# Kernel tuning notes

Hardware: AMD Instinct MI355X
Metric: run time of the kernel (lower is better)

Reference implementation:

```python
import jax, jax.numpy as jnp
import numpy as np
import math

SHIFTS = (1, 2, 4, 8)
EPS_IN = 1e-5  # InstanceNorm2d eps
EPS_BN = 1e-5  # BatchNorm2d eps

def _eight_shifts(x, d):
    # Reproduces DATrans.feature_padding: 8 reflection-padded shifted views.
    H, W = x.shape[-2], x.shape[-1]
    def p(rt, rb, cl, cr):
        return jnp.pad(x, ((0, 0), (0, 0), (rt, rb), (cl, cr)), mode='reflect')
    return [
        p(d, 0, d, 0)[..., :H, :W],   # left-top
        p(d, 0, 0, 0)[..., :H, :],    # center-top
        p(d, 0, 0, d)[..., :H, d:],   # right-top
        p(0, 0, d, 0)[..., :, :W],    # left-center
        p(0, 0, 0, d)[..., :, d:],    # right-center
        p(0, d, d, 0)[..., d:, :W],   # left-bottom
        p(0, d, 0, 0)[..., d:, :],    # center-bottom
        p(0, d, 0, d)[..., d:, d:],   # right-bottom
    ]

def _l2n(x):
    # torch F.normalize(dim=-1, eps=1e-12)
    return x / jnp.maximum(jnp.linalg.norm(x, axis=-1, keepdims=True), 1e-12)

def setup_inputs() -> dict:
    key = jax.random.key(0)
    ks = jax.random.split(key, 9)
    B, Cin, H, W = 4, 16, 256, 256
    heads, hidden, NL, Cout = 4, 16, 8, 16
    tra = heads * hidden
    cen = jax.random.normal(ks[0], (B, Cin, H, W), jnp.float32)
    q_w = jax.random.normal(ks[1], (heads, hidden, Cin), jnp.float32) / np.sqrt(Cin).astype(np.float32)
    k_w = jax.random.normal(ks[2], (heads, hidden * NL, Cin * NL), jnp.float32) / np.sqrt(Cin * NL).astype(np.float32)
    v_w = jax.random.normal(ks[3], (heads, hidden * NL, Cin * NL), jnp.float32) / np.sqrt(Cin * NL).astype(np.float32)
    out_w = jax.random.normal(ks[4], (Cout, tra), jnp.float32) / np.sqrt(tra).astype(np.float32)
    bn_gamma = jax.random.uniform(ks[5], (Cout,), jnp.float32) + 0.5
    bn_beta = jax.random.normal(ks[6], (Cout,), jnp.float32) * 0.1
    bn_mean = jax.random.normal(ks[7], (Cout,), jnp.float32) * 0.1
    bn_var = jax.random.uniform(ks[8], (Cout,), jnp.float32) + 0.5
    return dict(cen=cen, q_w=q_w, k_w=k_w, v_w=v_w, out_w=out_w,
                bn_gamma=bn_gamma, bn_beta=bn_beta, bn_mean=bn_mean, bn_var=bn_var)

def reference(cen, q_w, k_w, v_w, out_w, bn_gamma, bn_beta, bn_mean, bn_var):
    b, Cin, H, W = cen.shape
    area = H * W
    heads = len(SHIFTS)
    qs, ksl, vsl = [], [], []
    for i, d in enumerate(SHIFTS):  # small fixed loop over heads
        sur = jnp.concatenate([s - cen for s in _eight_shifts(cen, d)], axis=1)  # [b, 8*Cin, H, W]
        ksl.append(jnp.einsum('oc,bchw->bohw', k_w[i], sur))  # 1x1 conv, no bias
        vsl.append(jnp.einsum('oc,bchw->bohw', v_w[i], sur))
        qs.append(jnp.einsum('oc,bchw->bohw', q_w[i], cen))
    # torch stack(dim=2).view(b, heads, -1, area) on contiguous tensor == stack+reshape
    K = jnp.stack(ksl, axis=2).reshape(b, heads, -1, area)  # [b, heads, 8*hid, area]
    Q = jnp.stack(qs, axis=2).reshape(b, heads, -1, area)   # [b, heads, hid, area]
    V = jnp.stack(vsl, axis=2).reshape(b, heads, -1, area)
    scores = jnp.einsum('bhca,bhda->bhcd', _l2n(Q), _l2n(K)) / math.sqrt(area)  # [b,h,hid,8*hid]
    # InstanceNorm2d(heads): per (b, head) over last two dims, no affine
    mu = scores.mean(axis=(-2, -1), keepdims=True)
    var = scores.var(axis=(-2, -1), keepdims=True)
    attn = jax.nn.softmax((scores - mu) * jax.lax.rsqrt(var + EPS_IN), axis=-1)
    out = jnp.einsum('bhcd,bhda->bhca', attn, V)  # [b, heads, hid, area]
    tra = out.shape[1] * out.shape[2]
    out = out.reshape(b, tra, H, W)
    out = jnp.einsum('oc,bchw->bohw', out_w, out)  # out_conv 1x1, no bias
    g = bn_gamma[None, :, None, None]
    bta = bn_beta[None, :, None, None]
    m = bn_mean[None, :, None, None]
    v = bn_var[None, :, None, None]
    out = (out - m) * jax.lax.rsqrt(v + EPS_BN) * g + bta  # eval-mode BatchNorm2d
    return jax.nn.relu(out)
```

## Files before the change

### kernel.cpp

```cpp
#include <hip/hip_runtime.h>
#include <math.h>

#define HH 256
#define WW 256
#define AREA 65536
#define CIN 16
#define NS 4
#define CSUR 128
#define NEXT 144
#define NPAIR 45

typedef __attribute__((ext_vector_type(8))) _Float16 f16x8;
typedef __attribute__((ext_vector_type(4))) float f32x4;

__constant__ int c_dy[8] = {-1,-1,-1, 0, 0, 1, 1, 1};
__constant__ int c_dx[8] = {-1, 0, 1,-1, 1,-1, 0, 1};

__device__ constexpr int CTI[NPAIR] = {
    0, 1,1, 2,2,2, 3,3,3,3, 4,4,4,4,4,
    5,5,5,5,5,5, 6,6,6,6,6,6,6, 7,7,7,7,7,7,7,7,
    8,8,8,8,8,8,8,8,8};
__device__ constexpr int CTJ[NPAIR] = {
    0, 0,1, 0,1,2, 0,1,2,3, 0,1,2,3,4,
    0,1,2,3,4,5, 0,1,2,3,4,5,6, 0,1,2,3,4,5,6,7,
    0,1,2,3,4,5,6,7,8};

__device__ __forceinline__ int refl(int v) {
    return v < 0 ? -v : (v > 255 ? 510 - v : v);
}

__device__ __forceinline__ unsigned pkh(float a, float b) {
    auto h2 = __builtin_amdgcn_cvt_pkrtz(a, b);
    return __builtin_bit_cast(unsigned, h2);
}

__device__ __forceinline__ void wph(unsigned* __restrict__ m,
                                    int c, int pxp, int halfk, float a, float b) {
    const int sw = c & 7, gi = halfk * 4 + (pxp >> 2), e = pxp & 3;
    m[c * 32 + ((gi ^ sw) << 2) + e] = pkh(a, b);
}

template <bool FAST>
__device__ __forceinline__ void stage64(unsigned* __restrict__ m,
                                        const float* __restrict__ base,
                                        int y, int x0, int cin, int pxp, int d) {
    constexpr int DY[8] = {-1,-1,-1, 0, 0, 1, 1, 1};
    constexpr int DX[8] = {-1, 0, 1,-1, 1,-1, 0, 1};
    const int xA = x0 + 2 * pxp;
    const int xB = xA + 32;
    const float* rowy = base + y * WW;
    const float2 cA = *(const float2*)(rowy + xA);
    const float2 cB = *(const float2*)(rowy + xB);
    wph(m, cin, pxp, 0, cA.x, cA.y);
    wph(m, cin, pxp, 1, cB.x, cB.y);
#pragma unroll
    for (int kk = 0; kk < 8; ++kk) {
        float2 sA, sB;
        if (FAST) {
            const float* row = base + (y + DY[kk] * d) * WW;
            sA = *(const float2*)(row + xA + DX[kk] * d);
            sB = *(const float2*)(row + xB + DX[kk] * d);
        } else {
            const int ys = refl(y + DY[kk] * d);
            const float* row = base + ys * WW;
            const int off = DX[kk] * d;
            sA.x = row[refl(xA + off)];
            sA.y = row[refl(xA + 1 + off)];
            sB.x = row[refl(xB + off)];
            sB.y = row[refl(xB + 1 + off)];
        }
        const int c = 16 + kk * 16 + cin;
        wph(m, c, pxp, 0, sA.x - cA.x, sA.y - cA.y);
        wph(m, c, pxp, 1, sB.x - cB.x, sB.y - cB.y);
    }
}

__global__ __launch_bounds__(256) void k1_gram(const float* __restrict__ cen,
                                               float* __restrict__ part) {
    const int chunk = blockIdx.x;
    const int s = blockIdx.y;
    const int b = blockIdx.z;
    const int d = 1 << s;
    const int t = threadIdx.x;
    const int lane = t & 63, wid = t >> 6;
    const int lr = lane & 15, lg = lane >> 4;
    const int cin = t >> 4, pxp = t & 15;
    const int y0 = chunk * 4;
    const float* base = cen + ((size_t)b * CIN + cin) * AREA;

    __shared__ unsigned lds[NEXT * 32];

    const int rA = ((lg ^ (lr & 7)) << 2);
    const int rB = (((4 + lg) ^ (lr & 7)) << 2);

    f32x4 acc[12];
#pragma unroll
    for (int i = 0; i < 12; ++i) acc[i] = (f32x4){0.f, 0.f, 0.f, 0.f};

    for (int rd = 0; rd < 16; ++rd) {
        const int y  = y0 + (rd >> 2);
        const int x0 = (rd & 3) * 64;
        if (y >= 8 && y <= 247 && x0 >= 64 && x0 <= 128)
            stage64<true>(lds, base, y, x0, cin, pxp, d);
        else
            stage64<false>(lds, base, y, x0, cin, pxp, d);
        __syncthreads();
        f16x8 fA[9], fB[9];
#pragma unroll
        for (int tt = 0; tt < 9; ++tt) {
            const int rb = (tt * 16 + lr) * 32;
            fA[tt] = __builtin_bit_cast(f16x8, *(const uint4*)(lds + rb + rA));
            fB[tt] = __builtin_bit_cast(f16x8, *(const uint4*)(lds + rb + rB));
        }
        __syncthreads();
#pragma unroll
        for (int p = 0; p < NPAIR; ++p) {
            if ((p & 3) == wid) {
                const int i = CTI[p], j = CTJ[p], a = p >> 2;
                acc[a] = __builtin_amdgcn_mfma_f32_16x16x32_f16(fA[i], fA[j], acc[a], 0, 0, 0);
                acc[a] = __builtin_amdgcn_mfma_f32_16x16x32_f16(fB[i], fB[j], acc[a], 0, 0, 0);
            }
        }
    }

    float* tb = part + (size_t)((chunk & 3) * 16 + b * 4 + s) * 20736;
#pragma unroll
    for (int p = 0; p < NPAIR; ++p) {
        if ((p & 3) == wid) {
            const int gi0 = CTI[p] * 16 + lg * 4;
            const int gj  = CTJ[p] * 16 + lr;
            const f32x4 a = acc[p >> 2];
#pragma unroll
            for (int r = 0; r < 4; ++r)
                atomicAdd(&tb[(gi0 + r) * 144 + gj], a[r]);
        }
    }
}

__global__ __launch_bounds__(256) void kA(const float* __restrict__ part,
                                          const float* __restrict__ q_w,
                                          const float* __restrict__ k_w,
                                          float* __restrict__ A,
                                          float* __restrict__ normK,
                                          float* __restrict__ normQ) {
    const int s = blockIdx.x, b = blockIdx.y, z = blockIdx.z, bs = b * 4 + s;
    const int t = threadIdx.x;
    const int i0 = z * 16;
    __shared__ float Ts[16][148];
    __shared__ float kwS[128][129];
    __shared__ float red[2][128];

    const float* p0 = part + (size_t)(0 * 16 + bs) * 20736;
    const float* p1 = part + (size_t)(1 * 16 + bs) * 20736;
    const float* p2 = part + (size_t)(2 * 16 + bs) * 20736;
    const float* p3 = part + (size_t)(3 * 16 + bs) * 20736;
    for (int e = t; e < 16 * 144; e += 256) {
        const int il = e / 144, j = e - il * 144;
        const int i = i0 + il;
        const int src = (i >= j) ? (i * 144 + j) : (j * 144 + i);
        Ts[il][j] = p0[src] + p1[src] + p2[src] + p3[src];
    }
    if (z >= 1) {
        const float* kws = k_w + (size_t)s * 16384;
        for (int e = t; e < 16384; e += 256)
            kwS[e >> 7][e & 127] = kws[e];
    }
    __syncthreads();

    if (z >= 1) {
        for (int e = t; e < 1024; e += 256) {
            const int il = e >> 6, jq = e & 63;
            const float* qr = q_w + jq * 16;
            float aa = 0.f;
#pragma unroll
            for (int c = 0; c < 16; ++c) aa = fmaf(qr[c], Ts[il][c], aa);
            A[((size_t)bs * 64 + jq) * 128 + (i0 - 16 + il)] = aa;
        }
        const int ck = t & 127, half = t >> 7;
        float accil[16];
#pragma unroll
        for (int il = 0; il < 16; ++il) accil[il] = 0.f;
        for (int j = half * 64; j < half * 64 + 64; ++j) {
            const float kj = kwS[ck][j];
#pragma unroll
            for (int il = 0; il < 16; ++il)
                accil[il] = fmaf(kj, Ts[il][16 + j], accil[il]);
        }
        float prt = 0.f;
#pragma unroll
        for (int il = 0; il < 16; ++il)
            prt = fmaf(kwS[ck][i0 - 16 + il], accil[il], prt);
        red[half][ck] = prt;
        __syncthreads();
        if (t < 128)
            atomicAdd(&normK[(size_t)bs * 128 + t], red[0][t] + red[1][t]);
    } else if (s == 0 && t < 64) {
        float nq = 0.f;
#pragma unroll
        for (int c1 = 0; c1 < 16; ++c1) {
            float ra = 0.f;
#pragma unroll
            for (int c2 = 0; c2 < 16; ++c2)
                ra = fmaf(q_w[t * 16 + c2], Ts[c1][c2], ra);
            nq = fmaf(q_w[t * 16 + c1], ra, nq);
        }
        normQ[b * 64 + t] = nq;
    }
}

__global__ __launch_bounds__(256) void kB(const float* __restrict__ k_w,
                                          const float* __restrict__ v_w,
                                          const float* __restrict__ A,
                                          const float* __restrict__ normK,
                                          const float* __restrict__ normQ,
                                          float* __restrict__ wEff) {
    const int a = blockIdx.x, b = blockIdx.y;
    const int t = threadIdx.x;
    __shared__ float AS[4][16][128];
    __shared__ float kv[4][32][132];
    __shared__ float sc[2048];
    __shared__ float red[256];
    __shared__ float rowred[256];
    __shared__ float rowmax[16], rowsum[16];
    __shared__ float s_mu, s_rs;

    for (int idx = t; idx < 8192; idx += 256) {
        const int sk = idx >> 11, rr = (idx >> 7) & 15, cp = idx & 127;
        const int jq = (rr & 3) * 16 + 4 * a + (rr >> 2);
        AS[sk][rr][cp] = A[((size_t)(b * 4 + sk) * 64 + jq) * 128 + cp];
    }
    for (int idx = t; idx < 16384; idx += 256) {
        const int sk = idx >> 12, ckl = (idx >> 7) & 31, cp = idx & 127;
        kv[sk][ckl][cp] = k_w[((size_t)sk * 128 + 32 * a + ckl) * 128 + cp];
    }
    __syncthreads();
    for (int e = t; e < 2048; e += 256) {
        const int r = e >> 7, dd = e & 127;
        const int sk = dd & 3, ckl = dd >> 2;
        const float4* Ar = (const float4*)(&AS[sk][r][0]);
        const float4* kr = (const float4*)(&kv[sk][ckl][0]);
        float4 pv = {0.f, 0.f, 0.f, 0.f};
#pragma unroll 8
        for (int jj = 0; jj < 32; ++jj) {
            const float4 h = Ar[jj], k4 = kr[jj];
            pv.x = fmaf(h.x, k4.x, pv.x);
            pv.y = fmaf(h.y, k4.y, pv.y);
            pv.z = fmaf(h.z, k4.z, pv.z);
            pv.w = fmaf(h.w, k4.w, pv.w);
        }
        const float dot = pv.x + pv.y + pv.z + pv.w;
        const int jq = (r & 3) * 16 + 4 * a + (r >> 2);
        const float qn = fmaxf(sqrtf(fmaxf(normQ[b * 64 + jq], 0.f)), 1e-12f);
        const float kn = fmaxf(sqrtf(fmaxf(normK[(size_t)(b * 4 + sk) * 128 + 32 * a + ckl], 0.f)), 1e-12f);
        sc[e] = dot / (qn * kn * 256.0f);
    }
    __syncthreads();
    for (int idx = t; idx < 16384; idx += 256) {
        const int sk = idx >> 12, m = (idx >> 7) & 31, cp = idx & 127;
        kv[sk][m][cp] = v_w[((size_t)sk * 128 + 32 * a + m) * 128 + cp];
    }
    {
        float p = 0.f;
        for (int e = t; e < 2048; e += 256) p += sc[e];
        red[t] = p; __syncthreads();
        for (int off = 128; off > 0; off >>= 1) {
            if (t < off) red[t] += red[t + off];
            __syncthreads();
        }
        if (t == 0) s_mu = red[0] * (1.f / 2048.f);
        __syncthreads();
    }
    {
        const float mu = s_mu;
        float p = 0.f;
        for (int e = t; e < 2048; e += 256) { const float z = sc[e] - mu; p += z * z; }
        red[t] = p; __syncthreads();
        for (int off = 128; off > 0; off >>= 1) {
            if (t < off) red[t] += red[t + off];
            __syncthreads();
        }
        if (t == 0) s_rs = rsqrtf(red[0] * (1.f / 2048.f) + 1e-5f);
        __syncthreads();
    }
    const float mu = s_mu, rs = s_rs;
    const int r = t >> 4, l = t & 15;
    {
        float m = -1e30f;
#pragma unroll
        for (int j = 0; j < 8; ++j) {
            const float z = (sc[r * 128 + l + j * 16] - mu) * rs;
            m = fmaxf(m, z);
        }
        rowred[t] = m; __syncthreads();
        if (l == 0) {
            float m2 = rowred[r * 16];
            for (int j = 1; j < 16; ++j) m2 = fmaxf(m2, rowred[r * 16 + j]);
            rowmax[r] = m2;
        }
        __syncthreads();
    }
    {
        float p = 0.f;
#pragma unroll
        for (int j = 0; j < 8; ++j) {
            const float z = (sc[r * 128 + l + j * 16] - mu) * rs;
            p += expf(z - rowmax[r]);
        }
        rowred[t] = p; __syncthreads();
        if (l == 0) {
            float p2 = 0.f;
            for (int j = 0; j < 16; ++j) p2 += rowred[r * 16 + j];
            rowsum[r] = p2;
        }
        __syncthreads();
    }
    {
        float vals[8];
#pragma unroll
        for (int j = 0; j < 8; ++j) {
            const float z = (sc[r * 128 + l + j * 16] - mu) * rs;
            vals[j] = expf(z - rowmax[r]) / rowsum[r];
        }
        __syncthreads();
#pragma unroll
        for (int j = 0; j < 8; ++j) sc[r * 128 + l + j * 16] = vals[j];
        __syncthreads();
    }
    for (int e = t; e < 8192; e += 256) {
        const int sk = e >> 11, r2 = (e >> 7) & 15, cp = e & 127;
        float w = 0.f;
#pragma unroll
        for (int m = 0; m < 32; ++m)
            w = fmaf(sc[r2 * 128 + 4 * m + sk], kv[sk][m][cp], w);
        wEff[((size_t)(b * 4 + sk) * 64 + (a * 16 + r2)) * 128 + cp] = w;
    }
}

__global__ __launch_bounds__(256) void k2c(const float* __restrict__ out_w,
                                           const float* __restrict__ bn_gamma,
                                           const float* __restrict__ bn_var,
                                           const float* __restrict__ wEff,
                                           float* __restrict__ wFinT,
                                           float* __restrict__ wcG) {
    const int s = blockIdx.x, b = blockIdx.y;
    const int t = threadIdx.x;
    __shared__ float we[64][128];
    __shared__ float wfS[16][128];
    for (int idx = t; idx < 8192; idx += 256) {
        const int j = idx >> 7, cp = idx & 127;
        we[j][cp] = wEff[((size_t)(b * 4 + s) * 64 + j) * 128 + cp];
    }
    __syncthreads();
    for (int e = t; e < 2048; e += 256) {
        const int o = e >> 7, cp = e & 127;
        float w = 0.f;
#pragma unroll 16
        for (int j = 0; j < 64; ++j)
            w = fmaf(out_w[o * 64 + j], we[j][cp], w);
        const float scale = bn_gamma[o] * rsqrtf(bn_var[o] + 1e-5f);
        const float wv = w * scale;
        wfS[o][cp] = wv;
        wFinT[((size_t)(b * 4 + s) * 128 + cp) * 16 + o] = wv;
    }
    __syncthreads();
    {
        const int cin = t >> 4, o = t & 15;
        float p = 0.f;
#pragma unroll
        for (int kk = 0; kk < 8; ++kk) p += wfS[o][kk * 16 + cin];
        atomicAdd(&wcG[(size_t)b * 256 + cin * 16 + o], p);
    }
}

__global__ __launch_bounds__(256) void k3_out(const float* __restrict__ cen,
                                              const float* __restrict__ wFinT,
                                              const float* __restrict__ wcG,
                                              const float* __restrict__ bn_gamma,
                                              const float* __restrict__ bn_beta,
                                              const float* __restrict__ bn_mean,
                                              const float* __restrict__ bn_var,
                                              float* __restrict__ out) {
    const int y = blockIdx.x;
    const int b = blockIdx.y;
    const int x = threadIdx.x;
    const float* cb = cen + (size_t)b * CIN * AREA;

    float acc[16];
#pragma unroll
    for (int o = 0; o < 16; ++o) acc[o] = 0.f;

    for (int s = 0; s < NS; ++s) {
        const int d = 1 << s;
        for (int k = 0; k < 8; ++k) {
            const int ry = refl(y + c_dy[k] * d);
            const int rx = refl(x + c_dx[k] * d);
            const float* crow = cb + ry * WW;
            const int woff = __builtin_amdgcn_readfirstlane(
                ((b * 4 + s) * 128 + k * 16) * 16);
            const float* wbase = wFinT + woff;
#pragma unroll
            for (int cin = 0; cin < 16; ++cin) {
                const float v = crow[cin * AREA + rx];
                const float4* w4 = reinterpret_cast<const float4*>(wbase + cin * 16);
#pragma unroll
                for (int oq = 0; oq < 4; ++oq) {
                    const float4 w = w4[oq];
                    acc[oq*4+0] = fmaf(w.x, v, acc[oq*4+0]);
                    acc[oq*4+1] = fmaf(w.y, v, acc[oq*4+1]);
                    acc[oq*4+2] = fmaf(w.z, v, acc[oq*4+2]);
                    acc[oq*4+3] = fmaf(w.w, v, acc[oq*4+3]);
                }
            }
        }
    }
    {
        const float* crow = cb + y * WW;
        const int coff = __builtin_amdgcn_readfirstlane(b * 256);
        const float* wcb = wcG + coff;
#pragma unroll
        for (int cin = 0; cin < 16; ++cin) {
            const float v = crow[cin * AREA + x];
            const float4* w4 = reinterpret_cast<const float4*>(wcb + cin * 16);
#pragma unroll
            for (int oq = 0; oq < 4; ++oq) {
                const float4 w = w4[oq];
                acc[oq*4+0] = fmaf(-w.x, v, acc[oq*4+0]);
                acc[oq*4+1] = fmaf(-w.y, v, acc[oq*4+1]);
                acc[oq*4+2] = fmaf(-w.z, v, acc[oq*4+2]);
                acc[oq*4+3] = fmaf(-w.w, v, acc[oq*4+3]);
            }
        }
    }
#pragma unroll
    for (int o = 0; o < 16; ++o) {
        const float scale = bn_gamma[o] * rsqrtf(bn_var[o] + 1e-5f);
        const float bias  = bn_beta[o] - bn_mean[o] * scale;
        out[((size_t)(b * 16 + o) * HH + y) * WW + x] = fmaxf(acc[o] + bias, 0.f);
    }
}

extern "C" void kernel_launch(void* const* d_in, const int* in_sizes, int n_in,
                              void* d_out, int out_size, void* d_ws, size_t ws_size,
                              hipStream_t stream) {
    const float* cen      = (const float*)d_in[0];
    const float* q_w      = (const float*)d_in[1];
    const float* k_w      = (const float*)d_in[2];
    const float* v_w      = (const float*)d_in[3];
    const float* out_w    = (const float*)d_in[4];
    const float* bn_gamma = (const float*)d_in[5];
    const float* bn_beta  = (const float*)d_in[6];
    const float* bn_mean  = (const float*)d_in[7];
    const float* bn_var   = (const float*)d_in[8];
    float* out = (float*)d_out;

    char* ws = (char*)d_ws;
    const size_t PART_BYTES  = (size_t)4 * 16 * 20736 * 4;
    const size_t NK_BYTES    = (size_t)16 * 128 * 4;
    const size_t WC_BYTES    = (size_t)4 * 256 * 4;
    const size_t A_BYTES     = (size_t)16 * 64 * 128 * 4;
    const size_t NQ_BYTES    = (size_t)4 * 64 * 4;
    const size_t WEFF_BYTES  = (size_t)16 * 64 * 128 * 4;

    float* part  = (float*)(ws);
    float* normK = (float*)(ws + PART_BYTES);
    float* wcG   = (float*)(ws + PART_BYTES + NK_BYTES);
    float* A     = (float*)(ws + PART_BYTES + NK_BYTES + WC_BYTES);
    float* normQ = (float*)(ws + PART_BYTES + NK_BYTES + WC_BYTES + A_BYTES);
    float* wEff  = (float*)(ws + PART_BYTES + NK_BYTES + WC_BYTES + A_BYTES + NQ_BYTES);
    float* wFinT = (float*)(ws + PART_BYTES + NK_BYTES + WC_BYTES + A_BYTES + NQ_BYTES + WEFF_BYTES);

    (void)hipMemsetAsync(part, 0, PART_BYTES + NK_BYTES + WC_BYTES, stream);
    k1_gram<<<dim3(64, 4, 4), 256, 0, stream>>>(cen, part);
    kA<<<dim3(4, 4, 9), 256, 0, stream>>>(part, q_w, k_w, A, normK, normQ);
    kB<<<dim3(4, 4), 256, 0, stream>>>(k_w, v_w, A, normK, normQ, wEff);
    k2c<<<dim3(4, 4), 256, 0, stream>>>(out_w, bn_gamma, bn_var, wEff, wFinT, wcG);
    k3_out<<<dim3(256, 4), 256, 0, stream>>>(cen, wFinT, wcG, bn_gamma, bn_beta,
                                             bn_mean, bn_var, out);
}
```

Baseline: 256.6 us.

## Pack input to fp16 pairs and use dot2 in output kernel

Adds a pre-pass that packs the fp32 input into half2 channel pairs, along with packed fp16 weights, so the output kernel reads half the bytes per gathered neighbor and uses v_dot2 instead of scalar FMAs. It also shrinks the gram partial buffers from four slices to two, which cuts the memset and the reduction reads. The trade-offs are an extra full-tensor pack pass, lower precision in the output accumulation, and more atomic contention per slice.

```diff
diff --git a/kernel.cpp b/kernel.cpp
--- a/kernel.cpp
+++ b/kernel.cpp
@@ -11,6 +11,7 @@
 #define NPAIR 45
 
 typedef __attribute__((ext_vector_type(8))) _Float16 f16x8;
+typedef __attribute__((ext_vector_type(2))) _Float16 f16x2;
 typedef __attribute__((ext_vector_type(4))) float f32x4;
 
 __constant__ int c_dy[8] = {-1,-1,-1, 0, 0, 1, 1, 1};
@@ -32,6 +33,11 @@
 __device__ __forceinline__ unsigned pkh(float a, float b) {
     auto h2 = __builtin_amdgcn_cvt_pkrtz(a, b);
     return __builtin_bit_cast(unsigned, h2);
+}
+
+__device__ __forceinline__ float fdot2(unsigned v, unsigned w, float acc) {
+    return __builtin_amdgcn_fdot2(__builtin_bit_cast(f16x2, v),
+                                  __builtin_bit_cast(f16x2, w), acc, false);
 }
 
 __device__ __forceinline__ void wph(unsigned* __restrict__ m,
@@ -75,6 +81,17 @@
     }
 }
 
+__global__ __launch_bounds__(256) void k0_pack(const float* __restrict__ cen,
+                                               unsigned* __restrict__ cenH) {
+    const size_t i = (size_t)blockIdx.x * 256 + threadIdx.x;
+    const int b = (int)(i >> 19);
+    const int c2 = (int)((i >> 16) & 7);
+    const int pix = (int)(i & 65535);
+    const float a  = cen[((size_t)b * 16 + 2 * c2) * AREA + pix];
+    const float bb = cen[((size_t)b * 16 + 2 * c2 + 1) * AREA + pix];
+    cenH[i] = pkh(a, bb);
+}
+
 __global__ __launch_bounds__(256) void k1_gram(const float* __restrict__ cen,
                                                float* __restrict__ part) {
     const int chunk = blockIdx.x;
@@ -123,7 +140,7 @@
         }
     }
 
-    float* tb = part + (size_t)((chunk & 3) * 16 + b * 4 + s) * 20736;
+    float* tb = part + (size_t)((chunk & 1) * 16 + b * 4 + s) * 20736;
 #pragma unroll
     for (int p = 0; p < NPAIR; ++p) {
         if ((p & 3) == wid) {
@@ -152,13 +169,11 @@
 
     const float* p0 = part + (size_t)(0 * 16 + bs) * 20736;
     const float* p1 = part + (size_t)(1 * 16 + bs) * 20736;
-    const float* p2 = part + (size_t)(2 * 16 + bs) * 20736;
-    const float* p3 = part + (size_t)(3 * 16 + bs) * 20736;
     for (int e = t; e < 16 * 144; e += 256) {
         const int il = e / 144, j = e - il * 144;
         const int i = i0 + il;
         const int src = (i >= j) ? (i * 144 + j) : (j * 144 + i);
-        Ts[il][j] = p0[src] + p1[src] + p2[src] + p3[src];
+        Ts[il][j] = p0[src] + p1[src];
     }
     if (z >= 1) {
         const float* kws = k_w + (size_t)s * 16384;
@@ -340,7 +355,7 @@
                                            const float* __restrict__ bn_gamma,
                                            const float* __restrict__ bn_var,
                                            const float* __restrict__ wEff,
-                                           float* __restrict__ wFinT,
+                                           unsigned* __restrict__ wPk,
                                            float* __restrict__ wcG) {
     const int s = blockIdx.x, b = blockIdx.y;
     const int t = threadIdx.x;
@@ -358,11 +373,14 @@
         for (int j = 0; j < 64; ++j)
             w = fmaf(out_w[o * 64 + j], we[j][cp], w);
         const float scale = bn_gamma[o] * rsqrtf(bn_var[o] + 1e-5f);
-        const float wv = w * scale;
-        wfS[o][cp] = wv;
-        wFinT[((size_t)(b * 4 + s) * 128 + cp) * 16 + o] = wv;
+        wfS[o][cp] = w * scale;
     }
     __syncthreads();
+    for (int e = t; e < 1024; e += 256) {
+        const int k8 = e >> 7, c2 = (e >> 4) & 7, o = e & 15;
+        wPk[((size_t)(b * 4 + s) * 8 + k8) * 128 + c2 * 16 + o] =
+            pkh(wfS[o][k8 * 16 + 2 * c2], wfS[o][k8 * 16 + 2 * c2 + 1]);
+    }
     {
         const int cin = t >> 4, o = t & 15;
         float p = 0.f;
@@ -373,7 +391,8 @@
 }
 
 __global__ __launch_bounds__(256) void k3_out(const float* __restrict__ cen,
-                                              const float* __restrict__ wFinT,
+                                              const unsigned* __restrict__ cenH,
+                                              const unsigned* __restrict__ wPk,
                                               const float* __restrict__ wcG,
                                               const float* __restrict__ bn_gamma,
                                               const float* __restrict__ bn_beta,
@@ -383,7 +402,7 @@
     const int y = blockIdx.x;
     const int b = blockIdx.y;
     const int x = threadIdx.x;
-    const float* cb = cen + (size_t)b * CIN * AREA;
+    const unsigned* hb = cenH + (size_t)b * 8 * AREA;
 
     float acc[16];
 #pragma unroll
@@ -394,27 +413,27 @@
         for (int k = 0; k < 8; ++k) {
             const int ry = refl(y + c_dy[k] * d);
             const int rx = refl(x + c_dx[k] * d);
-            const float* crow = cb + ry * WW;
+            const unsigned* prow = hb + ry * WW + rx;
             const int woff = __builtin_amdgcn_readfirstlane(
-                ((b * 4 + s) * 128 + k * 16) * 16);
-            const float* wbase = wFinT + woff;
-#pragma unroll
-            for (int cin = 0; cin < 16; ++cin) {
-                const float v = crow[cin * AREA + rx];
-                const float4* w4 = reinterpret_cast<const float4*>(wbase + cin * 16);
+                ((b * 4 + s) * 8 + k) * 128);
+            const unsigned* wbase = wPk + woff;
+#pragma unroll
+            for (int c2 = 0; c2 < 8; ++c2) {
+                const unsigned v = prow[c2 * AREA];
+                const uint4* w4 = reinterpret_cast<const uint4*>(wbase + c2 * 16);
 #pragma unroll
                 for (int oq = 0; oq < 4; ++oq) {
-                    const float4 w = w4[oq];
-                    acc[oq*4+0] = fmaf(w.x, v, acc[oq*4+0]);
-                    acc[oq*4+1] = fmaf(w.y, v, acc[oq*4+1]);
-                    acc[oq*4+2] = fmaf(w.z, v, acc[oq*4+2]);
-                    acc[oq*4+3] = fmaf(w.w, v, acc[oq*4+3]);
+                    const uint4 wv = w4[oq];
+                    acc[oq*4+0] = fdot2(v, wv.x, acc[oq*4+0]);
+                    acc[oq*4+1] = fdot2(v, wv.y, acc[oq*4+1]);
+                    acc[oq*4+2] = fdot2(v, wv.z, acc[oq*4+2]);
+                    acc[oq*4+3] = fdot2(v, wv.w, acc[oq*4+3]);
                 }
             }
         }
     }
     {
-        const float* crow = cb + y * WW;
+        const float* crow = cen + (size_t)b * CIN * AREA + y * WW;
         const int coff = __builtin_amdgcn_readfirstlane(b * 256);
         const float* wcb = wcG + coff;
 #pragma unroll
@@ -454,26 +473,29 @@
     float* out = (float*)d_out;
 
     char* ws = (char*)d_ws;
-    const size_t PART_BYTES  = (size_t)4 * 16 * 20736 * 4;
+    const size_t PART_BYTES  = (size_t)2 * 16 * 20736 * 4;
     const size_t NK_BYTES    = (size_t)16 * 128 * 4;
     const size_t WC_BYTES    = (size_t)4 * 256 * 4;
     const size_t A_BYTES     = (size_t)16 * 64 * 128 * 4;
     const size_t NQ_BYTES    = (size_t)4 * 64 * 4;
     const size_t WEFF_BYTES  = (size_t)16 * 64 * 128 * 4;
-
-    float* part  = (float*)(ws);
-    float* normK = (float*)(ws + PART_BYTES);
-    float* wcG   = (float*)(ws + PART_BYTES + NK_BYTES);
-    float* A     = (float*)(ws + PART_BYTES + NK_BYTES + WC_BYTES);
-    float* normQ = (float*)(ws + PART_BYTES + NK_BYTES + WC_BYTES + A_BYTES);
-    float* wEff  = (float*)(ws + PART_BYTES + NK_BYTES + WC_BYTES + A_BYTES + NQ_BYTES);
-    float* wFinT = (float*)(ws + PART_BYTES + NK_BYTES + WC_BYTES + A_BYTES + NQ_BYTES + WEFF_BYTES);
+    const size_t WPK_BYTES   = (size_t)16 * 8 * 128 * 4;
+
+    float*    part  = (float*)(ws);
+    float*    normK = (float*)(ws + PART_BYTES);
+    float*    wcG   = (float*)(ws + PART_BYTES + NK_BYTES);
+    float*    A     = (float*)(ws + PART_BYTES + NK_BYTES + WC_BYTES);
+    float*    normQ = (float*)(ws + PART_BYTES + NK_BYTES + WC_BYTES + A_BYTES);
+    float*    wEff  = (float*)(ws + PART_BYTES + NK_BYTES + WC_BYTES + A_BYTES + NQ_BYTES);
+    unsigned* wPk   = (unsigned*)(ws + PART_BYTES + NK_BYTES + WC_BYTES + A_BYTES + NQ_BYTES + WEFF_BYTES);
+    unsigned* cenH  = (unsigned*)(ws + PART_BYTES + NK_BYTES + WC_BYTES + A_BYTES + NQ_BYTES + WEFF_BYTES + WPK_BYTES);
 
     (void)hipMemsetAsync(part, 0, PART_BYTES + NK_BYTES + WC_BYTES, stream);
+    k0_pack<<<dim3(8192), 256, 0, stream>>>(cen, cenH);
     k1_gram<<<dim3(64, 4, 4), 256, 0, stream>>>(cen, part);
     kA<<<dim3(4, 4, 9), 256, 0, stream>>>(part, q_w, k_w, A, normK, normQ);
     kB<<<dim3(4, 4), 256, 0, stream>>>(k_w, v_w, A, normK, normQ, wEff);
-    k2c<<<dim3(4, 4), 256, 0, stream>>>(out_w, bn_gamma, bn_var, wEff, wFinT, wcG);
-    k3_out<<<dim3(256, 4), 256, 0, stream>>>(cen, wFinT, wcG, bn_gamma, bn_beta,
-                                             bn_mean, bn_var, out);
-}
+    k2c<<<dim3(4, 4), 256, 0, stream>>>(out_w, bn_gamma, bn_var, wEff, wPk, wcG);
+    k3_out<<<dim3(256, 4), 256, 0, stream>>>(cen, cenH, wPk, wcG, bn_gamma,
+                                             bn_beta, bn_mean, bn_var, out);
+}
```

New measurement: 238.0 us (median of 2 runs). 1.08x faster.
